# Performance work log

Measured on AMD Instinct MI355X. Metric: run time of the kernel, lower is better.

## Reference

```python
import jax, jax.numpy as jnp
import numpy as np

B, T, C, H = 2, 2048, 1024, 16
HD = C // H  # 64

def setup_inputs() -> dict:
    key = jax.random.key(0)
    ks = jax.random.split(key, 9)
    s = 0.02
    return {
        "x": jax.random.normal(ks[0], (B, T, C), jnp.float32),
        "Wq": jax.random.normal(ks[1], (C, C), jnp.float32) * s,
        "bq": jax.random.normal(ks[2], (C,), jnp.float32) * s,
        "Wk": jax.random.normal(ks[3], (C, C), jnp.float32) * s,
        "bk": jax.random.normal(ks[4], (C,), jnp.float32) * s,
        "Wv": jax.random.normal(ks[5], (C, C), jnp.float32) * s,
        "bv": jax.random.normal(ks[6], (C,), jnp.float32) * s,
        "Wp": jax.random.normal(ks[7], (C, C), jnp.float32) * s,
        "bp": jax.random.normal(ks[8], (C,), jnp.float32) * s,
    }

def reference(x, Wq, bq, Wk, bk, Wv, bv, Wp, bp):
    Bb, Tt, Cc = x.shape
    hd = Cc // H
    # project and split heads: [B, H, T, hd]
    def heads(W, b):
        return (x @ W.T + b).reshape(Bb, Tt, H, hd).transpose(0, 2, 1, 3)
    q, k, v = heads(Wq, bq), heads(Wk, bk), heads(Wv, bv)
    scale = 1.0 / np.sqrt(hd).astype(np.float32)
    att = jnp.einsum('bhqd,bhkd->bhqk', q, k) * scale
    causal = jnp.tril(jnp.ones((Tt, Tt), bool))
    att = jnp.where(causal[None, None], att, -jnp.inf)
    att = jax.nn.softmax(att, axis=-1)
    y = jnp.einsum('bhqk,bhkd->bhqd', att, v)
    y = y.transpose(0, 2, 1, 3).reshape(Bb, Tt, Cc)
    return y @ Wp.T + bp
```

## Files before the change

kernel.cpp:

```cpp
#include <hip/hip_runtime.h>
#include <hip/hip_bf16.h>

#define Tsz 2048
#define Csz 1024
#define Hn 16

typedef short s8v __attribute__((ext_vector_type(8)));
typedef short s4v __attribute__((ext_vector_type(4)));
typedef float f4v __attribute__((ext_vector_type(4)));

#define QSCALE (0.125f * 1.44269504088896f)

__device__ __forceinline__ unsigned short bfr(float x) {
    return (unsigned short)((__builtin_bit_cast(unsigned, x) + 0x8000u) >> 16);
}
__device__ __forceinline__ unsigned pack2_rn(float a, float b) {
    const unsigned ua = __builtin_bit_cast(unsigned, a) + 0x8000u;
    const unsigned ub = __builtin_bit_cast(unsigned, b) + 0x8000u;
    return (ua >> 16) | (ub & 0xFFFF0000u);
}

__device__ __forceinline__ void gload_lds(const void* g, void* l) {
    __builtin_amdgcn_global_load_lds(
        (const __attribute__((address_space(1))) void*)g,
        (__attribute__((address_space(3))) void*)l, 16, 0, 0);
}

__global__ void cvt6(const float* __restrict__ x, const float* __restrict__ wq,
                     const float* __restrict__ wk, const float* __restrict__ wv,
                     const float* __restrict__ wp,
                     short* __restrict__ xo, short* __restrict__ qo,
                     short* __restrict__ ko, short* __restrict__ vo,
                     short* __restrict__ po) {
    const int bx = blockIdx.x;
    const float* in; short* out; int ib;
    if (bx < 4096) { in = x; out = xo; ib = bx; }
    else {
        const int r = bx - 4096, w = r >> 10;
        ib = r & 1023;
        switch (w) {
            case 0: in = wq; out = qo; break;
            case 1: in = wk; out = ko; break;
            case 2: in = wv; out = vo; break;
            default: in = wp; out = po; break;
        }
    }
    const int i = ib * 1024 + threadIdx.x * 4;
    float4 v = *(const float4*)(in + i);
    int2 o;
    o.x = (int)pack2_rn(v.x, v.y);
    o.y = (int)pack2_rn(v.z, v.w);
    *(int2*)(out + i) = o;
}

__global__ __launch_bounds__(256, 3) void qkv_gemm(
    const short* __restrict__ X,
    const short* __restrict__ Wq, const short* __restrict__ Wk, const short* __restrict__ Wv,
    const float* __restrict__ bq, const float* __restrict__ bk, const float* __restrict__ bv,
    short* __restrict__ Qo, short* __restrict__ Ko, short* __restrict__ Vto)
{
    const int z = blockIdx.z;
    const short* W = (z == 0) ? Wq : (z == 1) ? Wk : Wv;
    const float* bias = (z == 0) ? bq : (z == 1) ? bk : bv;

    __shared__ __align__(16) short Ash[128 * 32];
    __shared__ __align__(16) short Bsh[128 * 32];
    __shared__ __align__(16) short TR[64 * 72];

    const int tid = threadIdx.x, lane = tid & 63, wave = tid >> 6;
    const int ln = lane & 15, hi = lane >> 4;
    const int m0 = blockIdx.x * 128, n0 = blockIdx.y * 128;
    const int wm = (wave >> 1) * 64, wn = (wave & 1) * 64;

    const short* Ag = X + (size_t)(m0 + (tid >> 2)) * Csz + (tid & 3) * 8;
    const short* Bg = W + (size_t)(n0 + (tid >> 2)) * Csz + (tid & 3) * 8;

    f4v acc[4][4];
    #pragma unroll
    for (int mt = 0; mt < 4; mt++)
        #pragma unroll
        for (int nt = 0; nt < 4; nt++)
            #pragma unroll
            for (int i = 0; i < 4; i++) acc[mt][nt][i] = 0.f;

    for (int k0 = 0; k0 < Csz; k0 += 32) {
        __syncthreads();
        gload_lds(Ag + k0, Ash + tid * 8);
        gload_lds(Ag + k0 + (size_t)64 * Csz, Ash + 2048 + tid * 8);
        gload_lds(Bg + k0, Bsh + tid * 8);
        gload_lds(Bg + k0 + (size_t)64 * Csz, Bsh + 2048 + tid * 8);
        __syncthreads();

        s8v af[4], bfr_[4];
        #pragma unroll
        for (int mt = 0; mt < 4; mt++)
            af[mt] = *(const s8v*)(Ash + (wm + mt * 16 + ln) * 32 + hi * 8);
        #pragma unroll
        for (int nt = 0; nt < 4; nt++)
            bfr_[nt] = *(const s8v*)(Bsh + (wn + nt * 16 + ln) * 32 + hi * 8);
        #pragma unroll
        for (int mt = 0; mt < 4; mt++)
            #pragma unroll
            for (int nt = 0; nt < 4; nt++)
                acc[mt][nt] = __builtin_amdgcn_mfma_f32_16x16x32_bf16(af[mt], bfr_[nt], acc[mt][nt], 0, 0, 0);
    }

    if (z == 2) {
        const int b = m0 >> 11, t0 = m0 & 2047;
        float bvv[4];
        #pragma unroll
        for (int nt = 0; nt < 4; nt++) bvv[nt] = bias[n0 + wn + nt * 16 + ln];
        #pragma unroll
        for (int ph = 0; ph < 4; ph++) {
            const int mh = ph >> 1, nh = ph & 1;
            __syncthreads();
            if ((wave >> 1) == mh && (wave & 1) == nh) {
                #pragma unroll
                for (int mt = 0; mt < 4; mt++)
                    #pragma unroll
                    for (int nt = 0; nt < 4; nt++) {
                        int2 pk;
                        pk.x = (int)pack2_rn(acc[mt][nt][0] + bvv[nt], acc[mt][nt][1] + bvv[nt]);
                        pk.y = (int)pack2_rn(acc[mt][nt][2] + bvv[nt], acc[mt][nt][3] + bvv[nt]);
                        *(int2*)(TR + (nt * 16 + ln) * 72 + mt * 16 + hi * 4) = pk;
                    }
            }
            __syncthreads();
            const int chl = tid >> 2, seg = tid & 3;
            const s8v r0 = *(const s8v*)(TR + chl * 72 + seg * 16);
            const s8v r1 = *(const s8v*)(TR + chl * 72 + seg * 16 + 8);
            short* dst = Vto + (size_t)(b * 1024 + n0 + nh * 64 + chl) * Tsz + t0 + mh * 64 + seg * 16;
            *(s8v*)(dst) = r0;
            *(s8v*)(dst + 8) = r1;
        }
        return;
    }

    const float scale = (z == 0) ? QSCALE : 1.0f;
    short* out = (z == 0) ? Qo : Ko;

    #pragma unroll
    for (int nt = 0; nt < 4; nt++) {
        const int col = n0 + wn + nt * 16 + ln;
        const float bvv = bias[col];
        #pragma unroll
        for (int mt = 0; mt < 4; mt++) {
            const int row0 = m0 + wm + mt * 16 + hi * 4;
            #pragma unroll
            for (int i = 0; i < 4; i++)
                out[(size_t)(row0 + i) * Csz + col] = (short)bfr((acc[mt][nt][i] + bvv) * scale);
        }
    }
}

__global__ __launch_bounds__(256, 2) void proj_gemm(
    const short* __restrict__ A, const short* __restrict__ W,
    const float* __restrict__ bias, float* __restrict__ out)
{
    __shared__ __align__(16) short Ash[128 * 32];
    __shared__ __align__(16) short Bsh[64 * 32];

    const int tid = threadIdx.x, lane = tid & 63, wave = tid >> 6;
    const int ln = lane & 15, hi = lane >> 4;
    const int m0 = blockIdx.x * 128, n0 = blockIdx.y * 64;
    const int wm = (wave >> 1) * 64, wn = (wave & 1) * 32;

    const short* Ag = A + (size_t)(m0 + (tid >> 2)) * Csz + (tid & 3) * 8;
    const short* Bg = W + (size_t)(n0 + (tid >> 2)) * Csz + (tid & 3) * 8;

    f4v acc[4][2];
    #pragma unroll
    for (int mt = 0; mt < 4; mt++)
        #pragma unroll
        for (int nt = 0; nt < 2; nt++)
            #pragma unroll
            for (int i = 0; i < 4; i++) acc[mt][nt][i] = 0.f;

    for (int k0 = 0; k0 < Csz; k0 += 32) {
        __syncthreads();
        gload_lds(Ag + k0, Ash + tid * 8);
        gload_lds(Ag + k0 + (size_t)64 * Csz, Ash + 2048 + tid * 8);
        gload_lds(Bg + k0, Bsh + tid * 8);
        __syncthreads();

        s8v af[4], bfr_[2];
        #pragma unroll
        for (int mt = 0; mt < 4; mt++)
            af[mt] = *(const s8v*)(Ash + (wm + mt * 16 + ln) * 32 + hi * 8);
        #pragma unroll
        for (int nt = 0; nt < 2; nt++)
            bfr_[nt] = *(const s8v*)(Bsh + (wn + nt * 16 + ln) * 32 + hi * 8);
        #pragma unroll
        for (int mt = 0; mt < 4; mt++)
            #pragma unroll
            for (int nt = 0; nt < 2; nt++)
                acc[mt][nt] = __builtin_amdgcn_mfma_f32_16x16x32_bf16(af[mt], bfr_[nt], acc[mt][nt], 0, 0, 0);
    }

    #pragma unroll
    for (int nt = 0; nt < 2; nt++) {
        const int col = n0 + wn + nt * 16 + ln;
        const float bvv = bias[col];
        #pragma unroll
        for (int mt = 0; mt < 4; mt++)
            #pragma unroll
            for (int i = 0; i < 4; i++)
                out[(size_t)(m0 + wm + mt * 16 + hi * 4 + i) * Csz + col] = acc[mt][nt][i] + bvv;
    }
}

__global__ __launch_bounds__(256, 4) void attn10(
    const short* __restrict__ Q, const short* __restrict__ Kg,
    const short* __restrict__ Vt, short* __restrict__ Y)
{
    __shared__ __align__(16) short Ksh[64 * 72];
    __shared__ __align__(16) short Vsh[64 * 72];
    __shared__ __align__(16) short Psh[4][16 * 72];

    const int tid = threadIdx.x, lane = tid & 63, wave = tid >> 6;
    const int ln = lane & 15, hi = lane >> 4;

    const int n = blockIdx.x;
    const int c = n & 255, j = n >> 8;
    const int bh = (j << 3) | (c >> 5);
    const int t = c & 31;
    const int qt = (j & 1) ? t : 31 - t;

    const size_t base = (size_t)(bh >> 4) * Tsz * Csz + (size_t)(bh & 15) * 64;
    const size_t vtbase = (size_t)bh * 64 * Tsz;
    const int qrel = wave * 16 + ln;
    short* Pq = Psh[wave];

    s8v qf[2];
    #pragma unroll
    for (int kk = 0; kk < 2; kk++)
        qf[kk] = *(const s8v*)(Q + base + (size_t)(qt * 64 + qrel) * Csz + kk * 32 + hi * 8);

    f4v o[4];
    float lsum = 0.f;
    #pragma unroll
    for (int dt = 0; dt < 4; dt++)
        #pragma unroll
        for (int i = 0; i < 4; i++) o[dt][i] = 0.f;

    const int sr = tid >> 3, sc = (tid & 7) * 8;
    const short* Kp = Kg + base + (size_t)sr * Csz + sc;
    const short* Vp = Vt + vtbase + (size_t)sr * Tsz + sc;
    const int swo = sr * 72 + sc;
    const int nkb = qt + 1;

    s8v k0 = *(const s8v*)(Kp);
    s8v k1 = *(const s8v*)(Kp + (size_t)32 * Csz);
    s8v v0 = *(const s8v*)(Vp);
    s8v v1 = *(const s8v*)(Vp + (size_t)32 * Tsz);
    *(s8v*)(&Ksh[swo]) = k0;
    *(s8v*)(&Ksh[swo + 32 * 72]) = k1;
    *(s8v*)(&Vsh[swo]) = v0;
    *(s8v*)(&Vsh[swo + 32 * 72]) = v1;
    __syncthreads();

    for (int kb = 0; kb < nkb; kb++) {
        const bool more = (kb + 1 < nkb);
        if (more) {
            const size_t ko = (size_t)(kb + 1) * 64;
            k0 = *(const s8v*)(Kp + ko * Csz);
            k1 = *(const s8v*)(Kp + (ko + 32) * Csz);
            v0 = *(const s8v*)(Vp + ko);
            v1 = *(const s8v*)(Vp + ko + (size_t)32 * Tsz);
        }

        s8v kf[2][4], vf[2][4];
        #pragma unroll
        for (int nt = 0; nt < 4; nt++)
            #pragma unroll
            for (int kk = 0; kk < 2; kk++) {
                kf[kk][nt] = *(const s8v*)(&Ksh[(nt * 16 + ln) * 72 + kk * 32 + hi * 8]);
                vf[kk][nt] = *(const s8v*)(&Vsh[(nt * 16 + ln) * 72 + kk * 32 + hi * 8]);
            }

        f4v s[4];
        #pragma unroll
        for (int nt = 0; nt < 4; nt++) {
            #pragma unroll
            for (int i = 0; i < 4; i++) s[nt][i] = 0.f;
            s[nt] = __builtin_amdgcn_mfma_f32_16x16x32_bf16(kf[0][nt], qf[0], s[nt], 0, 0, 0);
            s[nt] = __builtin_amdgcn_mfma_f32_16x16x32_bf16(kf[1][nt], qf[1], s[nt], 0, 0, 0);
        }

        const bool dg = !more;
        #pragma unroll
        for (int nt = 0; nt < 4; nt++) {
            float pv[4];
            #pragma unroll
            for (int i = 0; i < 4; i++) pv[i] = exp2f(s[nt][i]);
            if (dg) {
                const int kr = nt * 16 + hi * 4;
                #pragma unroll
                for (int i = 0; i < 4; i++)
                    if (kr + i > qrel) pv[i] = 0.f;
            }
            lsum += (pv[0] + pv[1]) + (pv[2] + pv[3]);
            int2 w;
            w.x = (int)pack2_rn(pv[0], pv[1]);
            w.y = (int)pack2_rn(pv[2], pv[3]);
            *(int2*)(Pq + ln * 72 + nt * 16 + hi * 4) = w;
        }
        const s8v pb0 = *(const s8v*)(Pq + ln * 72 + hi * 8);
        const s8v pb1 = *(const s8v*)(Pq + ln * 72 + 32 + hi * 8);

        #pragma unroll
        for (int dt = 0; dt < 4; dt++) {
            o[dt] = __builtin_amdgcn_mfma_f32_16x16x32_bf16(vf[0][dt], pb0, o[dt], 0, 0, 0);
            o[dt] = __builtin_amdgcn_mfma_f32_16x16x32_bf16(vf[1][dt], pb1, o[dt], 0, 0, 0);
        }

        if (more) {
            __syncthreads();
            *(s8v*)(&Ksh[swo]) = k0;
            *(s8v*)(&Ksh[swo + 32 * 72]) = k1;
            *(s8v*)(&Vsh[swo]) = v0;
            *(s8v*)(&Vsh[swo + 32 * 72]) = v1;
            __syncthreads();
        }
    }

    float l = lsum;
    l += __shfl_xor(l, 16);
    l += __shfl_xor(l, 32);
    const float inv = 1.0f / l;
    const int qrow = qt * 64 + qrel;
    #pragma unroll
    for (int dt = 0; dt < 4; dt++) {
        int2 w;
        w.x = (int)pack2_rn(o[dt][0] * inv, o[dt][1] * inv);
        w.y = (int)pack2_rn(o[dt][2] * inv, o[dt][3] * inv);
        *(int2*)(Y + base + (size_t)qrow * Csz + dt * 16 + hi * 4) = w;
    }
}

extern "C" void kernel_launch(void* const* d_in, const int* in_sizes, int n_in,
                              void* d_out, int out_size, void* d_ws, size_t ws_size,
                              hipStream_t stream) {
    const float* x  = (const float*)d_in[0];
    const float* Wq = (const float*)d_in[1];
    const float* bq = (const float*)d_in[2];
    const float* Wk = (const float*)d_in[3];
    const float* bk = (const float*)d_in[4];
    const float* Wv = (const float*)d_in[5];
    const float* bv = (const float*)d_in[6];
    const float* Wp = (const float*)d_in[7];
    const float* bp = (const float*)d_in[8];

    char* ws = (char*)d_ws;
    short* Xb  = (short*)(ws);
    short* Wqb = (short*)(ws + (8u  << 20));
    short* Wkb = (short*)(ws + (10u << 20));
    short* Wvb = (short*)(ws + (12u << 20));
    short* Wpb = (short*)(ws + (14u << 20));
    short* Qb  = (short*)(ws + (16u << 20));
    short* Kb  = (short*)(ws + (24u << 20));
    short* Vtb = (short*)(ws + (32u << 20));
    short* Yb  = (short*)(ws + (40u << 20));

    hipLaunchKernelGGL(cvt6, dim3(8192), dim3(256), 0, stream,
                       x, Wq, Wk, Wv, Wp, Xb, Wqb, Wkb, Wvb, Wpb);

    hipLaunchKernelGGL(qkv_gemm, dim3(32, 8, 3), dim3(256), 0, stream,
                       Xb, Wqb, Wkb, Wvb, bq, bk, bv, Qb, Kb, Vtb);

    hipLaunchKernelGGL(attn10, dim3(1024), dim3(256), 0, stream, Qb, Kb, Vtb, Yb);

    hipLaunchKernelGGL(proj_gemm, dim3(32, 16), dim3(256), 0, stream, Yb, Wpb, bp, (float*)d_out);
}
```

Baseline: 191.0 us.

## Software-pipeline PV MFMA one tile behind QK and XOR-swizzle K/V LDS

The attention kernel now defers the P·V MFMAs for each key block to the next iteration. They are issued right after the next block's Q·K MFMAs, which lets softmax/exp work overlap with matrix ops. P is double-buffered in LDS and V fragments are held in registers across the barrier. K/V shared tiles drop the 72-element padding in favour of an XOR swizzle, which cuts LDS footprint. The cost is extra register pressure from carrying vprev, plus a larger P buffer.

```diff
diff --git a/kernel.cpp b/kernel.cpp
--- a/kernel.cpp
+++ b/kernel.cpp
@@ -209,13 +209,13 @@
     }
 }
 
-__global__ __launch_bounds__(256, 4) void attn10(
+__global__ __launch_bounds__(256, 4) void attn13(
     const short* __restrict__ Q, const short* __restrict__ Kg,
     const short* __restrict__ Vt, short* __restrict__ Y)
 {
-    __shared__ __align__(16) short Ksh[64 * 72];
-    __shared__ __align__(16) short Vsh[64 * 72];
-    __shared__ __align__(16) short Psh[4][16 * 72];
+    __shared__ __align__(16) short Ksh[64 * 64];
+    __shared__ __align__(16) short Vsh[64 * 64];
+    __shared__ __align__(16) short Psh[2][4][16 * 72];
 
     const int tid = threadIdx.x, lane = tid & 63, wave = tid >> 6;
     const int ln = lane & 15, hi = lane >> 4;
@@ -229,7 +229,6 @@
     const size_t base = (size_t)(bh >> 4) * Tsz * Csz + (size_t)(bh & 15) * 64;
     const size_t vtbase = (size_t)bh * 64 * Tsz;
     const int qrel = wave * 16 + ln;
-    short* Pq = Psh[wave];
 
     s8v qf[2];
     #pragma unroll
@@ -243,21 +242,30 @@
         #pragma unroll
         for (int i = 0; i < 4; i++) o[dt][i] = 0.f;
 
-    const int sr = tid >> 3, sc = (tid & 7) * 8;
-    const short* Kp = Kg + base + (size_t)sr * Csz + sc;
-    const short* Vp = Vt + vtbase + (size_t)sr * Tsz + sc;
-    const int swo = sr * 72 + sc;
+    const int sr = tid >> 3, scs = tid & 7;
+    const short* Kp = Kg + base + (size_t)sr * Csz + scs * 8;
+    const short* Vp = Vt + vtbase + (size_t)sr * Tsz + scs * 8;
+    const int swo = sr * 64 + (scs ^ (sr & 7)) * 8;
     const int nkb = qt + 1;
+
+    int foff[2][4];
+    #pragma unroll
+    for (int nt = 0; nt < 4; nt++)
+        #pragma unroll
+        for (int kk = 0; kk < 2; kk++)
+            foff[kk][nt] = (nt * 16 + ln) * 64 + (((kk * 4 + hi) ^ (ln & 7)) * 8);
 
     s8v k0 = *(const s8v*)(Kp);
     s8v k1 = *(const s8v*)(Kp + (size_t)32 * Csz);
     s8v v0 = *(const s8v*)(Vp);
     s8v v1 = *(const s8v*)(Vp + (size_t)32 * Tsz);
     *(s8v*)(&Ksh[swo]) = k0;
-    *(s8v*)(&Ksh[swo + 32 * 72]) = k1;
+    *(s8v*)(&Ksh[swo + 32 * 64]) = k1;
     *(s8v*)(&Vsh[swo]) = v0;
-    *(s8v*)(&Vsh[swo + 32 * 72]) = v1;
+    *(s8v*)(&Vsh[swo + 32 * 64]) = v1;
     __syncthreads();
+
+    s8v vprev[2][4];
 
     for (int kb = 0; kb < nkb; kb++) {
         const bool more = (kb + 1 < nkb);
@@ -269,14 +277,12 @@
             v1 = *(const s8v*)(Vp + ko + (size_t)32 * Tsz);
         }
 
-        s8v kf[2][4], vf[2][4];
+        s8v kf[2][4];
         #pragma unroll
         for (int nt = 0; nt < 4; nt++)
             #pragma unroll
-            for (int kk = 0; kk < 2; kk++) {
-                kf[kk][nt] = *(const s8v*)(&Ksh[(nt * 16 + ln) * 72 + kk * 32 + hi * 8]);
-                vf[kk][nt] = *(const s8v*)(&Vsh[(nt * 16 + ln) * 72 + kk * 32 + hi * 8]);
-            }
+            for (int kk = 0; kk < 2; kk++)
+                kf[kk][nt] = *(const s8v*)(&Ksh[foff[kk][nt]]);
 
         f4v s[4];
         #pragma unroll
@@ -287,7 +293,19 @@
             s[nt] = __builtin_amdgcn_mfma_f32_16x16x32_bf16(kf[1][nt], qf[1], s[nt], 0, 0, 0);
         }
 
+        if (kb > 0) {
+            const short* Pr = Psh[(kb - 1) & 1][wave];
+            const s8v pb0 = *(const s8v*)(Pr + ln * 72 + hi * 8);
+            const s8v pb1 = *(const s8v*)(Pr + ln * 72 + 32 + hi * 8);
+            #pragma unroll
+            for (int dt = 0; dt < 4; dt++) {
+                o[dt] = __builtin_amdgcn_mfma_f32_16x16x32_bf16(vprev[0][dt], pb0, o[dt], 0, 0, 0);
+                o[dt] = __builtin_amdgcn_mfma_f32_16x16x32_bf16(vprev[1][dt], pb1, o[dt], 0, 0, 0);
+            }
+        }
+
         const bool dg = !more;
+        short* Pw = Psh[kb & 1][wave];
         #pragma unroll
         for (int nt = 0; nt < 4; nt++) {
             float pv[4];
@@ -303,24 +321,33 @@
             int2 w;
             w.x = (int)pack2_rn(pv[0], pv[1]);
             w.y = (int)pack2_rn(pv[2], pv[3]);
-            *(int2*)(Pq + ln * 72 + nt * 16 + hi * 4) = w;
-        }
-        const s8v pb0 = *(const s8v*)(Pq + ln * 72 + hi * 8);
-        const s8v pb1 = *(const s8v*)(Pq + ln * 72 + 32 + hi * 8);
-
-        #pragma unroll
-        for (int dt = 0; dt < 4; dt++) {
-            o[dt] = __builtin_amdgcn_mfma_f32_16x16x32_bf16(vf[0][dt], pb0, o[dt], 0, 0, 0);
-            o[dt] = __builtin_amdgcn_mfma_f32_16x16x32_bf16(vf[1][dt], pb1, o[dt], 0, 0, 0);
-        }
+            *(int2*)(Pw + ln * 72 + nt * 16 + hi * 4) = w;
+        }
+
+        #pragma unroll
+        for (int nt = 0; nt < 4; nt++)
+            #pragma unroll
+            for (int kk = 0; kk < 2; kk++)
+                vprev[kk][nt] = *(const s8v*)(&Vsh[foff[kk][nt]]);
 
         if (more) {
             __syncthreads();
             *(s8v*)(&Ksh[swo]) = k0;
-            *(s8v*)(&Ksh[swo + 32 * 72]) = k1;
+            *(s8v*)(&Ksh[swo + 32 * 64]) = k1;
             *(s8v*)(&Vsh[swo]) = v0;
-            *(s8v*)(&Vsh[swo + 32 * 72]) = v1;
+            *(s8v*)(&Vsh[swo + 32 * 64]) = v1;
             __syncthreads();
+        }
+    }
+
+    {
+        const short* Pr = Psh[(nkb - 1) & 1][wave];
+        const s8v pb0 = *(const s8v*)(Pr + ln * 72 + hi * 8);
+        const s8v pb1 = *(const s8v*)(Pr + ln * 72 + 32 + hi * 8);
+        #pragma unroll
+        for (int dt = 0; dt < 4; dt++) {
+            o[dt] = __builtin_amdgcn_mfma_f32_16x16x32_bf16(vprev[0][dt], pb0, o[dt], 0, 0, 0);
+            o[dt] = __builtin_amdgcn_mfma_f32_16x16x32_bf16(vprev[1][dt], pb1, o[dt], 0, 0, 0);
         }
     }
 
@@ -368,7 +395,7 @@
     hipLaunchKernelGGL(qkv_gemm, dim3(32, 8, 3), dim3(256), 0, stream,
                        Xb, Wqb, Wkb, Wvb, bq, bk, bv, Qb, Kb, Vtb);
 
-    hipLaunchKernelGGL(attn10, dim3(1024), dim3(256), 0, stream, Qb, Kb, Vtb, Yb);
+    hipLaunchKernelGGL(attn13, dim3(1024), dim3(256), 0, stream, Qb, Kb, Vtb, Yb);
 
     hipLaunchKernelGGL(proj_gemm, dim3(32, 16), dim3(256), 0, stream, Yb, Wpb, bp, (float*)d_out);
 }
```

After: 196.6 us. 1.03x slower.
